# Kernel tuning notes

Measured on AMD Instinct MI355X. Metric: run time of the kernel, lower is better.

## Reference

```python
import jax, jax.numpy as jnp
import numpy as np

BATCH = 4194304
ACT_DIM = 8


def setup_inputs() -> dict:
    key = jax.random.key(0)
    x = jax.random.normal(key, (BATCH, ACT_DIM), dtype=jnp.float32)
    # clamp_params = [[lower, upper]] exactly as in the torch module
    clamp_params = jnp.array([[-0.15, 0.15]], dtype=jnp.float32)
    return {"x": x, "clamp_params": clamp_params}


def reference(x, clamp_params):
    # CVXPY layer solves: argmin_y ||y - x||^2  s.t.  lo <= y <= hi
    # whose exact solution is the box projection (clamp).
    lo = clamp_params[:, 0:1]  # [1,1] broadcasts over [B, A]
    hi = clamp_params[:, 1:2]
    return jnp.clip(x, lo, hi)
```

## Files before the change

### kernel.cpp

```cpp
#include <hip/hip_runtime.h>


typedef float f32x4 __attribute__((ext_vector_type(4)));

#define PT 8
#define BLOCK 256

__device__ __forceinline__ f32x4 clamp4(f32x4 v, float lo, float hi) {
    v.x = fminf(fmaxf(v.x, lo), hi);
    v.y = fminf(fmaxf(v.y, lo), hi);
    v.z = fminf(fmaxf(v.z, lo), hi);
    v.w = fminf(fmaxf(v.w, lo), hi);
    return v;
}

__global__ void __launch_bounds__(BLOCK) clamp_kernel(
    const f32x4* __restrict__ x,
    const float* __restrict__ cp,
    f32x4* __restrict__ out,
    int n4)
{
    const float lo = cp[0];
    const float hi = cp[1];
    const int base = blockIdx.x * (BLOCK * PT) + threadIdx.x;

    if (base + (PT - 1) * BLOCK < n4) {
        f32x4 v[PT];
#pragma unroll
        for (int k = 0; k < PT; ++k)
            v[k] = x[base + k * BLOCK];
#pragma unroll
        for (int k = 0; k < PT; ++k)
            out[base + k * BLOCK] = clamp4(v[k], lo, hi);
    } else {
#pragma unroll
        for (int k = 0; k < PT; ++k) {
            int idx = base + k * BLOCK;
            if (idx < n4)
                out[idx] = clamp4(x[idx], lo, hi);
        }
    }
}

extern "C" void kernel_launch(void* const* d_in, const int* in_sizes, int n_in,
                              void* d_out, int out_size, void* d_ws, size_t ws_size,
                              hipStream_t stream)
{
    const f32x4* x = (const f32x4*)d_in[0];
    const float* cp = (const float*)d_in[1];
    f32x4* out = (f32x4*)d_out;

    const int n = in_sizes[0];
    const int n4 = n / 4;

    const int per_block = BLOCK * PT;
    const int grid = (n4 + per_block - 1) / per_block;

    clamp_kernel<<<grid, BLOCK, 0, stream>>>(x, cp, out, n4);
}
```

Measured before the change: 228.2 us.

## Use persistent grid-stride kernel with software-pipelined double-buffered loads

Replaces the one-shot grid, where each thread processes 8 vectors, with a fixed grid of 1024 blocks that strides over the array. Each thread loads the next group of 4 vectors before storing the current group, and a sched_barrier keeps that order. The aim is to keep loads in flight across iterations and to avoid the cost of launching and scheduling thousands of blocks. The risk is less memory-level parallelism, since fewer waves are resident than a full grid would provide on a 256-CU chip.

```diff
diff --git a/kernel.cpp b/kernel.cpp
--- a/kernel.cpp
+++ b/kernel.cpp
@@ -3,8 +3,8 @@
 
 typedef float f32x4 __attribute__((ext_vector_type(4)));
 
-#define PT 8
 #define BLOCK 256
+#define ILP 4
 
 __device__ __forceinline__ f32x4 clamp4(f32x4 v, float lo, float hi) {
     v.x = fminf(fmaxf(v.x, lo), hi);
@@ -22,24 +22,41 @@
 {
     const float lo = cp[0];
     const float hi = cp[1];
-    const int base = blockIdx.x * (BLOCK * PT) + threadIdx.x;
 
-    if (base + (PT - 1) * BLOCK < n4) {
-        f32x4 v[PT];
+    const int nthreads = gridDim.x * BLOCK;
+    const int big = nthreads * ILP;
+    const int tid = blockIdx.x * BLOCK + threadIdx.x;
+    const int ngroups = n4 / big;
+
+    if (ngroups > 0) {
+        int i = tid;
+        f32x4 cur[ILP];
 #pragma unroll
-        for (int k = 0; k < PT; ++k)
-            v[k] = x[base + k * BLOCK];
+        for (int k = 0; k < ILP; ++k)
+            cur[k] = x[i + k * nthreads];
+
+        for (int g = 1; g < ngroups; ++g) {
+            const int inext = i + big;
+            f32x4 nxt[ILP];
 #pragma unroll
-        for (int k = 0; k < PT; ++k)
-            out[base + k * BLOCK] = clamp4(v[k], lo, hi);
-    } else {
+            for (int k = 0; k < ILP; ++k)
+                nxt[k] = x[inext + k * nthreads];
+            __builtin_amdgcn_sched_barrier(0);
 #pragma unroll
-        for (int k = 0; k < PT; ++k) {
-            int idx = base + k * BLOCK;
-            if (idx < n4)
-                out[idx] = clamp4(x[idx], lo, hi);
+            for (int k = 0; k < ILP; ++k)
+                out[i + k * nthreads] = clamp4(cur[k], lo, hi);
+#pragma unroll
+            for (int k = 0; k < ILP; ++k)
+                cur[k] = nxt[k];
+            i = inext;
         }
+#pragma unroll
+        for (int k = 0; k < ILP; ++k)
+            out[i + k * nthreads] = clamp4(cur[k], lo, hi);
     }
+
+    for (int idx = ngroups * big + tid; idx < n4; idx += nthreads)
+        out[idx] = clamp4(x[idx], lo, hi);
 }
 
 extern "C" void kernel_launch(void* const* d_in, const int* in_sizes, int n_in,
@@ -53,8 +70,10 @@
     const int n = in_sizes[0];
     const int n4 = n / 4;
 
-    const int per_block = BLOCK * PT;
-    const int grid = (n4 + per_block - 1) / per_block;
+    int grid = 1024;
+    const int needed = (n4 + BLOCK - 1) / BLOCK;
+    if (grid > needed) grid = needed;
+    if (grid < 1) grid = 1;
 
     clamp_kernel<<<grid, BLOCK, 0, stream>>>(x, cp, out, n4);
 }
```

New measurement: 236.8 us. 1.04x slower.
